# Performance work log

Measured on AMD Instinct MI355X. Metric: run time of the kernel, lower is better.

Reference implementation:

```python
import jax, jax.numpy as jnp
import numpy as np

N = 50000      # num nodes
E = 800000     # num edges (avg degree 16)
D_IN = 128
D_H = 128


def setup_inputs() -> dict:
    key = jax.random.key(0)
    k_x, k_e, k_w1, k_w2 = jax.random.split(key, 4)
    x = jax.random.normal(k_x, (N, D_IN), dtype=jnp.float32)
    edge_index = jax.random.randint(k_e, (2, E), 0, N, dtype=jnp.int64)
    s = 1.0 / np.sqrt(D_IN)  # glorot-ish scale
    W1 = jax.random.normal(k_w1, (D_IN, D_H), dtype=jnp.float32) * s
    W2 = jax.random.normal(k_w2, (D_H, D_H), dtype=jnp.float32) * s
    b1 = jnp.zeros((D_H,), dtype=jnp.float32)
    b2 = jnp.zeros((D_H,), dtype=jnp.float32)
    return {"x": x, "edge_index": edge_index, "W1": W1, "b1": b1, "W2": W2, "b2": b2}


def gcn_layer(x, src, dst, W, b, n):
    # PyG GCNConv: transform, add self-loops, sym-normalized scatter-add aggregation.
    h = x @ W                                            # [N, D]
    deg = jnp.zeros((n,), h.dtype).at[dst].add(1.0) + 1.0  # +1 = self-loop
    dinv = jax.lax.rsqrt(deg)                            # deg >= 1, safe
    norm = dinv[src] * dinv[dst]                         # [E]
    agg = jnp.zeros_like(h).at[dst].add(h[src] * norm[:, None])
    agg = agg + h * (dinv * dinv)[:, None]               # self-loop contribution
    return agg + b


def reference(x, edge_index, W1, b1, W2, b2):
    src, dst = edge_index[0], edge_index[1]
    h = gcn_layer(x, src, dst, W1, b1, N)
    h = jax.nn.relu(h)
    # dropout is identity in eval mode (training=False)
    return gcn_layer(h, src, dst, W2, b2, N)
```

## Files before the change

### kernel.cpp

```cpp
#include <hip/hip_runtime.h>

#define N_NODES 50000
#define N_EDGES 800000
#define D 128
#define NBUCK 196
#define CAP 8192
#define WT_LD 136

typedef float    f32x4 __attribute__((ext_vector_type(4)));
typedef _Float16 f16x4 __attribute__((ext_vector_type(4)));
typedef _Float16 half8 __attribute__((ext_vector_type(8)));

__device__ inline f32x4 cvt4(f16x4 h) {
    f32x4 r;
    r.x = (float)h.x; r.y = (float)h.y; r.z = (float)h.z; r.w = (float)h.w;
    return r;
}

__device__ inline half8 cvt8(const float* __restrict__ p) {
    f32x4 a = *(const f32x4*)p;
    f32x4 b = *(const f32x4*)(p + 4);
    half8 r;
    r[0] = (_Float16)a.x; r[1] = (_Float16)a.y; r[2] = (_Float16)a.z; r[3] = (_Float16)a.w;
    r[4] = (_Float16)b.x; r[5] = (_Float16)b.y; r[6] = (_Float16)b.z; r[7] = (_Float16)b.w;
    return r;
}


__global__ void k_zero(int* __restrict__ p, int n) {
    int i = blockIdx.x * blockDim.x + threadIdx.x;
    if (i < n) p[i] = 0;
}

__global__ __launch_bounds__(256) void k_bucket(const int* __restrict__ ei,
                                                int* __restrict__ gcur,
                                                int* __restrict__ pk) {
    __shared__ int lcnt[NBUCK];
    __shared__ int lbase[NBUCK];
    const int t = threadIdx.x;
    for (int i = t; i < NBUCK; i += 256) lcnt[i] = 0;
    __syncthreads();

    const int base = blockIdx.x * 2048;
    int  vals[8], bks[8], rks[8];
    bool ok[8];
#pragma unroll
    for (int u = 0; u < 8; ++u) {
        int e = base + u * 256 + t;
        ok[u] = (e < N_EDGES);
        if (ok[u]) {
            int s = ei[e];
            int d = ei[N_EDGES + e];
            bks[u]  = d >> 8;
            vals[u] = s | ((d & 255) << 16);
            rks[u]  = atomicAdd(&lcnt[bks[u]], 1);
        }
    }
    __syncthreads();
    for (int i = t; i < NBUCK; i += 256)
        lbase[i] = lcnt[i] ? atomicAdd(&gcur[i], lcnt[i]) : 0;
    __syncthreads();
#pragma unroll
    for (int u = 0; u < 8; ++u)
        if (ok[u])
            pk[bks[u] * CAP + lbase[bks[u]] + rks[u]] = vals[u];
}

__global__ __launch_bounds__(256) void k_csr(const int* __restrict__ gcur,
                                             const int* __restrict__ pk,
                                             int* __restrict__ rowstart,
                                             int* __restrict__ rowcnt,
                                             float* __restrict__ dinv,
                                             int* __restrict__ esrc) {
    __shared__ int hcnt[256];
    __shared__ int sbase[256];
    __shared__ int lcur[256];
    __shared__ int sd[256];
    __shared__ int lesrc[CAP];

    const int b  = blockIdx.x;
    const int t  = threadIdx.x;
    const int RB = b * CAP;
    const int nb = gcur[b];

    hcnt[t] = 0;
    lcur[t] = 0;
    __syncthreads();
    for (int i = t; i < nb; i += 256) {
        int dl = (pk[RB + i] >> 16) & 255;
        atomicAdd(&hcnt[dl], 1);
    }
    __syncthreads();

    int v = hcnt[t];
    sd[t] = v;
    __syncthreads();
    for (int off = 1; off < 256; off <<= 1) {
        int u = (t >= off) ? sd[t - off] : 0;
        __syncthreads();
        sd[t] += u;
        __syncthreads();
    }
    sbase[t] = sd[t] - v;
    __syncthreads();

    int g = b * 256 + t;
    if (g < N_NODES) {
        rowstart[g] = RB + sbase[t];
        rowcnt[g]   = v;
        dinv[g]     = rsqrtf((float)v + 1.0f);
    }

    for (int i = t; i < nb; i += 256) {
        int val = pk[RB + i];
        int dl  = (val >> 16) & 255;
        int r   = atomicAdd(&lcur[dl], 1);
        lesrc[sbase[dl] + r] = val & 0xFFFF;
    }
    __syncthreads();
    for (int i = t; i < nb; i += 256)
        esrc[RB + i] = lesrc[i];
}


template <typename XT>
__global__ __launch_bounds__(256) void k_gemm(const XT* __restrict__ X,
                                              const float* __restrict__ W,
                                              const float* __restrict__ dinv,
                                              _Float16* __restrict__ H) {
    __shared__ __align__(16) _Float16 WT[128 * WT_LD];

    const int tid  = threadIdx.x;
    const int base = blockIdx.x * 64;
    const int w    = tid >> 6;
    const int lane = tid & 63;
    const int c    = lane & 15;
    const int g    = lane >> 4;

    for (int idx = tid; idx < 128 * 128; idx += 256) {
        int k = idx >> 7, cc = idx & 127;
        WT[cc * WT_LD + k] = (_Float16)W[idx];
    }
    __syncthreads();

    half8 bf[8][4];
#pragma unroll
    for (int n = 0; n < 8; ++n)
#pragma unroll
        for (int t = 0; t < 4; ++t)
            bf[n][t] = *(const half8*)&WT[(n * 16 + c) * WT_LD + t * 32 + g * 8];
    __syncthreads();

    int rowA = base + w * 16 + c;
    if (rowA >= N_NODES) rowA = N_NODES - 1;
    half8 af[4];
#pragma unroll
    for (int t = 0; t < 4; ++t) {
        if constexpr (sizeof(XT) == 2)
            af[t] = *(const half8*)(X + (size_t)rowA * D + t * 32 + g * 8);
        else
            af[t] = cvt8((const float*)X + (size_t)rowA * D + t * 32 + g * 8);
    }

    f32x4 acc[8];
#pragma unroll
    for (int n = 0; n < 8; ++n) acc[n] = (f32x4)0.f;
#pragma unroll
    for (int t = 0; t < 4; ++t)
#pragma unroll
        for (int n = 0; n < 8; ++n)
            acc[n] = __builtin_amdgcn_mfma_f32_16x16x32_f16(af[t], bf[n][t], acc[n], 0, 0, 0);

    float dv[4];
#pragma unroll
    for (int j = 0; j < 4; ++j) {
        int rr = base + w * 16 + g * 4 + j;
        dv[j] = dinv[rr < N_NODES ? rr : N_NODES - 1];
    }
#pragma unroll
    for (int n = 0; n < 8; ++n)
#pragma unroll
        for (int j = 0; j < 4; ++j)
            WT[(w * 16 + g * 4 + j) * WT_LD + n * 16 + c] = (_Float16)(acc[n][j] * dv[j]);
    __syncthreads();

    for (int idx = tid; idx < 64 * 16; idx += 256) {
        int r = idx >> 4, ch = idx & 15;
        int gr = base + r;
        if (gr < N_NODES)
            *(half8*)(H + (size_t)gr * D + ch * 8) = *(const half8*)&WT[r * WT_LD + ch * 8];
    }
}


template <int RELU, typename OT>
__global__ __launch_bounds__(256) void k_agg(const _Float16* __restrict__ Hs,
                                             const int* __restrict__ rowstart,
                                             const int* __restrict__ rowcnt,
                                             const int* __restrict__ esrc,
                                             const float* __restrict__ dinv,
                                             const float* __restrict__ bias,
                                             OT* __restrict__ OUT) {
    int node = blockIdx.x * 8 + (threadIdx.x >> 5);
    int lane = threadIdx.x & 31;
    const f16x4* Hv = (const f16x4*)Hs;

    float di = dinv[node];
    f32x4 acc = cvt4(Hv[(size_t)node * 32 + lane]);

    int s   = __builtin_nontemporal_load(&rowstart[node]);
    int cnt = __builtin_nontemporal_load(&rowcnt[node]);
    int e   = s + cnt;
    for (int off = s; off < e; off += 32) {
        int n = e - off;
        if (n > 32) n = 32;
        int idx  = off + (lane < n ? lane : n - 1);
        int eidx = __builtin_nontemporal_load(&esrc[idx]);
        int j = 0;
        for (; j + 7 < n; j += 8) {
            int s0 = __shfl(eidx, j, 32);
            int s1 = __shfl(eidx, j + 1, 32);
            int s2 = __shfl(eidx, j + 2, 32);
            int s3 = __shfl(eidx, j + 3, 32);
            int s4 = __shfl(eidx, j + 4, 32);
            int s5 = __shfl(eidx, j + 5, 32);
            int s6 = __shfl(eidx, j + 6, 32);
            int s7 = __shfl(eidx, j + 7, 32);
            f16x4 v0 = Hv[(size_t)s0 * 32 + lane];
            f16x4 v1 = Hv[(size_t)s1 * 32 + lane];
            f16x4 v2 = Hv[(size_t)s2 * 32 + lane];
            f16x4 v3 = Hv[(size_t)s3 * 32 + lane];
            f16x4 v4 = Hv[(size_t)s4 * 32 + lane];
            f16x4 v5 = Hv[(size_t)s5 * 32 + lane];
            f16x4 v6 = Hv[(size_t)s6 * 32 + lane];
            f16x4 v7 = Hv[(size_t)s7 * 32 + lane];
            acc += ((cvt4(v0) + cvt4(v1)) + (cvt4(v2) + cvt4(v3)))
                 + ((cvt4(v4) + cvt4(v5)) + (cvt4(v6) + cvt4(v7)));
        }
        for (; j + 3 < n; j += 4) {
            int s0 = __shfl(eidx, j, 32);
            int s1 = __shfl(eidx, j + 1, 32);
            int s2 = __shfl(eidx, j + 2, 32);
            int s3 = __shfl(eidx, j + 3, 32);
            f16x4 v0 = Hv[(size_t)s0 * 32 + lane];
            f16x4 v1 = Hv[(size_t)s1 * 32 + lane];
            f16x4 v2 = Hv[(size_t)s2 * 32 + lane];
            f16x4 v3 = Hv[(size_t)s3 * 32 + lane];
            acc += (cvt4(v0) + cvt4(v1)) + (cvt4(v2) + cvt4(v3));
        }
        for (; j < n; ++j) {
            int s0 = __shfl(eidx, j, 32);
            acc += cvt4(Hv[(size_t)s0 * 32 + lane]);
        }
    }

    f32x4 b = ((const f32x4*)bias)[lane];
    f32x4 r = acc * di + b;
    if (RELU) {
        r.x = fmaxf(r.x, 0.f);
        r.y = fmaxf(r.y, 0.f);
        r.z = fmaxf(r.z, 0.f);
        r.w = fmaxf(r.w, 0.f);
    }
    if constexpr (sizeof(OT) == 2) {
        f16x4 o;
        o.x = (_Float16)r.x; o.y = (_Float16)r.y;
        o.z = (_Float16)r.z; o.w = (_Float16)r.w;
        __builtin_nontemporal_store(o, (f16x4*)OUT + (size_t)node * 32 + lane);
    } else {
        __builtin_nontemporal_store(r, (f32x4*)OUT + (size_t)node * 32 + lane);
    }
}


extern "C" void kernel_launch(void* const* d_in, const int* in_sizes, int n_in,
                              void* d_out, int out_size, void* d_ws, size_t ws_size,
                              hipStream_t stream) {
    const float* x  = (const float*)d_in[0];
    const int*   ei = (const int*)d_in[1];
    const float* W1 = (const float*)d_in[2];
    const float* b1 = (const float*)d_in[3];
    const float* W2 = (const float*)d_in[4];
    const float* b2 = (const float*)d_in[5];
    float* out = (float*)d_out;

    int*      gcur     = (int*)d_ws;
    int*      rowstart = gcur + 256;
    int*      rowcnt   = rowstart + 50048;
    float*    dinv     = (float*)(rowcnt + 50048);
    int*      pk       = (int*)(dinv + 50048);
    int*      esrc     = pk + NBUCK * CAP;
    _Float16* h1       = (_Float16*)(esrc + NBUCK * CAP);
    _Float16* ag16     = h1 + 6400000;
    _Float16* h2       = ag16 + 6400000;

    const int TB  = 256;
    const int gbB = (N_EDGES + 2047) / 2048;
    const int gbG = (N_NODES + 63) / 64;

    k_zero<<<1, TB, 0, stream>>>(gcur, NBUCK);
    k_bucket<<<gbB, TB, 0, stream>>>(ei, gcur, pk);
    k_csr<<<NBUCK, TB, 0, stream>>>(gcur, pk, rowstart, rowcnt, dinv, esrc);

    k_gemm<float><<<gbG, TB, 0, stream>>>(x, W1, dinv, h1);
    k_agg<1, _Float16><<<N_NODES / 8, TB, 0, stream>>>(h1, rowstart, rowcnt, esrc, dinv, b1, ag16);
    k_gemm<_Float16><<<gbG, TB, 0, stream>>>(ag16, W2, dinv, h2);
    k_agg<0, float><<<N_NODES / 8, TB, 0, stream>>>(h2, rowstart, rowcnt, esrc, dinv, b2, out);
}
```

Baseline: 125.0 us.

## Split feature matrices into column planes for cache-local gather aggregation

Intermediate fp16 feature matrices are stored as four planes of 32 columns each, and the aggregation grid is split so each block handles one plane for 16 nodes. A block's gathers then touch a 3.2 MB plane instead of the full 12.8 MB matrix, which should improve L2/LLC hit rates for the random neighbor reads. The cost is four times as many edge-index and rowstart reads, narrower 4-byte gathers per lane, and extra blocks. The zeroing kernel is also replaced with hipMemsetAsync.

```diff
diff --git a/kernel.cpp b/kernel.cpp
--- a/kernel.cpp
+++ b/kernel.cpp
@@ -6,16 +6,12 @@
 #define NBUCK 196
 #define CAP 8192
 #define WT_LD 136
+#define PLANE_HALVES 1600000
 
 typedef float    f32x4 __attribute__((ext_vector_type(4)));
-typedef _Float16 f16x4 __attribute__((ext_vector_type(4)));
+typedef float    f32x2 __attribute__((ext_vector_type(2)));
+typedef _Float16 f16x2 __attribute__((ext_vector_type(2)));
 typedef _Float16 half8 __attribute__((ext_vector_type(8)));
-
-__device__ inline f32x4 cvt4(f16x4 h) {
-    f32x4 r;
-    r.x = (float)h.x; r.y = (float)h.y; r.z = (float)h.z; r.w = (float)h.w;
-    return r;
-}
 
 __device__ inline half8 cvt8(const float* __restrict__ p) {
     f32x4 a = *(const f32x4*)p;
@@ -26,11 +22,6 @@
     return r;
 }
 
-
-__global__ void k_zero(int* __restrict__ p, int n) {
-    int i = blockIdx.x * blockDim.x + threadIdx.x;
-    if (i < n) p[i] = 0;
-}
 
 __global__ __launch_bounds__(256) void k_bucket(const int* __restrict__ ei,
                                                 int* __restrict__ gcur,
@@ -157,7 +148,7 @@
 #pragma unroll
     for (int t = 0; t < 4; ++t) {
         if constexpr (sizeof(XT) == 2)
-            af[t] = *(const half8*)(X + (size_t)rowA * D + t * 32 + g * 8);
+            af[t] = *(const half8*)(X + (size_t)t * PLANE_HALVES + (size_t)rowA * 32 + g * 8);
         else
             af[t] = cvt8((const float*)X + (size_t)rowA * D + t * 32 + g * 8);
     }
@@ -184,91 +175,102 @@
             WT[(w * 16 + g * 4 + j) * WT_LD + n * 16 + c] = (_Float16)(acc[n][j] * dv[j]);
     __syncthreads();
 
-    for (int idx = tid; idx < 64 * 16; idx += 256) {
-        int r = idx >> 4, ch = idx & 15;
-        int gr = base + r;
+#pragma unroll
+    for (int ch = 0; ch < 4; ++ch) {
+        int r   = tid >> 2;
+        int sub = tid & 3;
+        int gr  = base + r;
         if (gr < N_NODES)
-            *(half8*)(H + (size_t)gr * D + ch * 8) = *(const half8*)&WT[r * WT_LD + ch * 8];
+            *(half8*)(H + (size_t)ch * PLANE_HALVES + (size_t)gr * 32 + sub * 8)
+                = *(const half8*)&WT[r * WT_LD + ch * 32 + sub * 8];
     }
 }
 
 
 template <int RELU, typename OT>
-__global__ __launch_bounds__(256) void k_agg(const _Float16* __restrict__ Hs,
+__global__ __launch_bounds__(256) void k_agg(const _Float16* __restrict__ Hq,
                                              const int* __restrict__ rowstart,
                                              const int* __restrict__ rowcnt,
                                              const int* __restrict__ esrc,
                                              const float* __restrict__ dinv,
                                              const float* __restrict__ bias,
                                              OT* __restrict__ OUT) {
-    int node = blockIdx.x * 8 + (threadIdx.x >> 5);
-    int lane = threadIdx.x & 31;
-    const f16x4* Hv = (const f16x4*)Hs;
+    const int chunk = blockIdx.x & 3;
+    const int grp   = threadIdx.x >> 4;
+    const int l     = threadIdx.x & 15;
+    const int node  = (blockIdx.x >> 2) * 16 + grp;
+    const _Float16* P = Hq + (size_t)chunk * PLANE_HALVES;
 
     float di = dinv[node];
-    f32x4 acc = cvt4(Hv[(size_t)node * 32 + lane]);
+    f16x2 h0 = *(const f16x2*)(P + (size_t)node * 32 + l * 2);
+    float a0 = (float)h0.x, a1 = (float)h0.y;
 
     int s   = __builtin_nontemporal_load(&rowstart[node]);
     int cnt = __builtin_nontemporal_load(&rowcnt[node]);
     int e   = s + cnt;
-    for (int off = s; off < e; off += 32) {
+    for (int off = s; off < e; off += 16) {
         int n = e - off;
-        if (n > 32) n = 32;
-        int idx  = off + (lane < n ? lane : n - 1);
+        if (n > 16) n = 16;
+        int idx  = off + (l < n ? l : n - 1);
         int eidx = __builtin_nontemporal_load(&esrc[idx]);
         int j = 0;
         for (; j + 7 < n; j += 8) {
-            int s0 = __shfl(eidx, j, 32);
-            int s1 = __shfl(eidx, j + 1, 32);
-            int s2 = __shfl(eidx, j + 2, 32);
-            int s3 = __shfl(eidx, j + 3, 32);
-            int s4 = __shfl(eidx, j + 4, 32);
-            int s5 = __shfl(eidx, j + 5, 32);
-            int s6 = __shfl(eidx, j + 6, 32);
-            int s7 = __shfl(eidx, j + 7, 32);
-            f16x4 v0 = Hv[(size_t)s0 * 32 + lane];
-            f16x4 v1 = Hv[(size_t)s1 * 32 + lane];
-            f16x4 v2 = Hv[(size_t)s2 * 32 + lane];
-            f16x4 v3 = Hv[(size_t)s3 * 32 + lane];
-            f16x4 v4 = Hv[(size_t)s4 * 32 + lane];
-            f16x4 v5 = Hv[(size_t)s5 * 32 + lane];
-            f16x4 v6 = Hv[(size_t)s6 * 32 + lane];
-            f16x4 v7 = Hv[(size_t)s7 * 32 + lane];
-            acc += ((cvt4(v0) + cvt4(v1)) + (cvt4(v2) + cvt4(v3)))
-                 + ((cvt4(v4) + cvt4(v5)) + (cvt4(v6) + cvt4(v7)));
+            int s0 = __shfl(eidx, j,     16);
+            int s1 = __shfl(eidx, j + 1, 16);
+            int s2 = __shfl(eidx, j + 2, 16);
+            int s3 = __shfl(eidx, j + 3, 16);
+            int s4 = __shfl(eidx, j + 4, 16);
+            int s5 = __shfl(eidx, j + 5, 16);
+            int s6 = __shfl(eidx, j + 6, 16);
+            int s7 = __shfl(eidx, j + 7, 16);
+            f16x2 v0 = *(const f16x2*)(P + (size_t)s0 * 32 + l * 2);
+            f16x2 v1 = *(const f16x2*)(P + (size_t)s1 * 32 + l * 2);
+            f16x2 v2 = *(const f16x2*)(P + (size_t)s2 * 32 + l * 2);
+            f16x2 v3 = *(const f16x2*)(P + (size_t)s3 * 32 + l * 2);
+            f16x2 v4 = *(const f16x2*)(P + (size_t)s4 * 32 + l * 2);
+            f16x2 v5 = *(const f16x2*)(P + (size_t)s5 * 32 + l * 2);
+            f16x2 v6 = *(const f16x2*)(P + (size_t)s6 * 32 + l * 2);
+            f16x2 v7 = *(const f16x2*)(P + (size_t)s7 * 32 + l * 2);
+            a0 += ((float)v0.x + (float)v1.x) + (((float)v2.x + (float)v3.x)
+                + (((float)v4.x + (float)v5.x) + ((float)v6.x + (float)v7.x)));
+            a1 += ((float)v0.y + (float)v1.y) + (((float)v2.y + (float)v3.y)
+                + (((float)v4.y + (float)v5.y) + ((float)v6.y + (float)v7.y)));
         }
         for (; j + 3 < n; j += 4) {
-            int s0 = __shfl(eidx, j, 32);
-            int s1 = __shfl(eidx, j + 1, 32);
-            int s2 = __shfl(eidx, j + 2, 32);
-            int s3 = __shfl(eidx, j + 3, 32);
-            f16x4 v0 = Hv[(size_t)s0 * 32 + lane];
-            f16x4 v1 = Hv[(size_t)s1 * 32 + lane];
-            f16x4 v2 = Hv[(size_t)s2 * 32 + lane];
-            f16x4 v3 = Hv[(size_t)s3 * 32 + lane];
-            acc += (cvt4(v0) + cvt4(v1)) + (cvt4(v2) + cvt4(v3));
+            int s0 = __shfl(eidx, j,     16);
+            int s1 = __shfl(eidx, j + 1, 16);
+            int s2 = __shfl(eidx, j + 2, 16);
+            int s3 = __shfl(eidx, j + 3, 16);
+            f16x2 v0 = *(const f16x2*)(P + (size_t)s0 * 32 + l * 2);
+            f16x2 v1 = *(const f16x2*)(P + (size_t)s1 * 32 + l * 2);
+            f16x2 v2 = *(const f16x2*)(P + (size_t)s2 * 32 + l * 2);
+            f16x2 v3 = *(const f16x2*)(P + (size_t)s3 * 32 + l * 2);
+            a0 += ((float)v0.x + (float)v1.x) + ((float)v2.x + (float)v3.x);
+            a1 += ((float)v0.y + (float)v1.y) + ((float)v2.y + (float)v3.y);
         }
         for (; j < n; ++j) {
-            int s0 = __shfl(eidx, j, 32);
-            acc += cvt4(Hv[(size_t)s0 * 32 + lane]);
+            int s0 = __shfl(eidx, j, 16);
+            f16x2 v0 = *(const f16x2*)(P + (size_t)s0 * 32 + l * 2);
+            a0 += (float)v0.x;
+            a1 += (float)v0.y;
         }
     }
 
-    f32x4 b = ((const f32x4*)bias)[lane];
-    f32x4 r = acc * di + b;
+    f32x2 bv = *(const f32x2*)(bias + chunk * 32 + l * 2);
+    float r0 = a0 * di + bv.x;
+    float r1 = a1 * di + bv.y;
     if (RELU) {
-        r.x = fmaxf(r.x, 0.f);
-        r.y = fmaxf(r.y, 0.f);
-        r.z = fmaxf(r.z, 0.f);
-        r.w = fmaxf(r.w, 0.f);
+        r0 = fmaxf(r0, 0.f);
+        r1 = fmaxf(r1, 0.f);
     }
     if constexpr (sizeof(OT) == 2) {
-        f16x4 o;
-        o.x = (_Float16)r.x; o.y = (_Float16)r.y;
-        o.z = (_Float16)r.z; o.w = (_Float16)r.w;
-        __builtin_nontemporal_store(o, (f16x4*)OUT + (size_t)node * 32 + lane);
+        f16x2 o;
+        o.x = (_Float16)r0; o.y = (_Float16)r1;
+        *(f16x2*)((_Float16*)OUT + (size_t)chunk * PLANE_HALVES + (size_t)node * 32 + l * 2) = o;
     } else {
-        __builtin_nontemporal_store(r, (f32x4*)OUT + (size_t)node * 32 + lane);
+        f32x2 o;
+        o.x = r0; o.y = r1;
+        __builtin_nontemporal_store(o, (f32x2*)((float*)OUT + (size_t)node * D + chunk * 32 + l * 2));
     }
 }
 
@@ -291,19 +293,20 @@
     int*      pk       = (int*)(dinv + 50048);
     int*      esrc     = pk + NBUCK * CAP;
     _Float16* h1       = (_Float16*)(esrc + NBUCK * CAP);
-    _Float16* ag16     = h1 + 6400000;
-    _Float16* h2       = ag16 + 6400000;
+    _Float16* ag16     = h1 + 4 * PLANE_HALVES;
+    _Float16* h2       = ag16 + 4 * PLANE_HALVES;
 
     const int TB  = 256;
     const int gbB = (N_EDGES + 2047) / 2048;
     const int gbG = (N_NODES + 63) / 64;
-
-    k_zero<<<1, TB, 0, stream>>>(gcur, NBUCK);
+    const int gbA = 4 * (N_NODES / 16);
+
+    hipMemsetAsync(gcur, 0, NBUCK * sizeof(int), stream);
     k_bucket<<<gbB, TB, 0, stream>>>(ei, gcur, pk);
     k_csr<<<NBUCK, TB, 0, stream>>>(gcur, pk, rowstart, rowcnt, dinv, esrc);
 
     k_gemm<float><<<gbG, TB, 0, stream>>>(x, W1, dinv, h1);
-    k_agg<1, _Float16><<<N_NODES / 8, TB, 0, stream>>>(h1, rowstart, rowcnt, esrc, dinv, b1, ag16);
+    k_agg<1, _Float16><<<gbA, TB, 0, stream>>>(h1, rowstart, rowcnt, esrc, dinv, b1, ag16);
     k_gemm<_Float16><<<gbG, TB, 0, stream>>>(ag16, W2, dinv, h2);
-    k_agg<0, float><<<N_NODES / 8, TB, 0, stream>>>(h2, rowstart, rowcnt, esrc, dinv, b2, out);
-}
+    k_agg<0, float><<<gbA, TB, 0, stream>>>(h2, rowstart, rowcnt, esrc, dinv, b2, out);
+}
```

Result: slower. 164.5 us (+31.7%).
